# Performance work log

Measured on AMD Instinct MI355X. Metric: run time of the kernel, lower is better.

The kernel has to match this reference:

```python
import jax, jax.numpy as jnp
import numpy as np

B, S, D = 2, 2048, 1024
H = 16
HD = D // H  # 64
SCALE = HD ** -0.5
EPS = 1e-12  # F.normalize eps


def _rope_sin_cos(length, half, dtype):
    positions = jnp.arange(length, dtype=dtype)
    freqs = jnp.arange(half, dtype=dtype)
    inv_freq = 1.0 / 10000 ** (freqs / max(1, half))
    theta = jnp.einsum('s,f->sf', positions, inv_freq)  # [S, half]
    return jnp.sin(theta)[None, None], jnp.cos(theta)[None, None]  # [1,1,S,half]


def _rotate(x, sin, cos):
    # x: [B,H,S,HD]; interleaved even/odd rotation
    x_even = x[..., 0::2]
    x_odd = x[..., 1::2]
    r_even = x_even * cos - x_odd * sin
    r_odd = x_even * sin + x_odd * cos
    return jnp.stack([r_even, r_odd], axis=-1).reshape(x.shape)


def setup_inputs() -> dict:
    key = jax.random.key(0)
    k1, k2, k3 = jax.random.split(key, 3)
    tokens = jax.random.normal(k1, (B, S, D), dtype=jnp.float32)
    qkv_w = jax.random.normal(k2, (3 * D, D), dtype=jnp.float32) * (D ** -0.5)
    qkv_b = jnp.zeros((3 * D,), dtype=jnp.float32)
    out_w = jax.random.normal(k3, (D, D), dtype=jnp.float32) * (D ** -0.5)
    out_b = jnp.zeros((D,), dtype=jnp.float32)
    return {"tokens": tokens, "qkv_w": qkv_w, "qkv_b": qkv_b,
            "out_w": out_w, "out_b": out_b}


def reference(tokens, qkv_w, qkv_b, out_w, out_b):
    batch, length, _ = tokens.shape
    qkv = tokens @ qkv_w.T + qkv_b                       # [B,S,3D]
    qkv = qkv.reshape(batch, length, 3, H, HD)
    qkv = jnp.transpose(qkv, (0, 3, 1, 2, 4))            # [B,H,S,3,HD]
    q, k, v = qkv[..., 0, :], qkv[..., 1, :], qkv[..., 2, :]
    sin, cos = _rope_sin_cos(length, HD // 2, q.dtype)
    q = _rotate(q, sin, cos)
    k = _rotate(k, sin, cos)
    # QK L2-normalize (F.normalize: x / max(||x||, eps))
    q = q / jnp.maximum(jnp.linalg.norm(q, axis=-1, keepdims=True), EPS)
    k = k / jnp.maximum(jnp.linalg.norm(k, axis=-1, keepdims=True), EPS)
    scores = jnp.einsum('bhqd,bhkd->bhqk', q, k) * SCALE
    attn = jax.nn.softmax(scores, axis=-1)
    out = jnp.einsum('bhqk,bhkd->bhqd', attn, v)          # [B,H,S,HD]
    out = jnp.transpose(out, (0, 2, 1, 3)).reshape(batch, length, D)
    return out @ out_w.T + out_b
```

## Files before the change

kernel.cpp:

```cpp
#include <hip/hip_runtime.h>
#include <hip/hip_bf16.h>
#include <math.h>

#define B_ 2
#define S_ 2048
#define D_ 1024
#define H_ 16
#define HD_ 64
#define BHS (B_*H_*S_)
#define NROWS (B_*S_)

typedef __attribute__((ext_vector_type(8))) short bf16x8;
typedef __attribute__((ext_vector_type(4))) short bf16x4;
typedef __attribute__((ext_vector_type(4))) float f32x4;
typedef __attribute__((ext_vector_type(4))) int i32x4;

#ifdef __HIP_DEVICE_COMPILE__
#define EXP2(x) __builtin_amdgcn_exp2f(x)
#else
#define EXP2(x) exp2f(x)
#endif

#define MFMA32(a, b, c) __builtin_amdgcn_mfma_f32_16x16x32_bf16(a, b, c, 0, 0, 0)

#define SCALE_LOG2E 0.18033688011112043f

#define VMCNT(N) asm volatile("s_waitcnt vmcnt(" #N ")" ::: "memory")
#define SBAR() do { __builtin_amdgcn_s_barrier(); \
                    __builtin_amdgcn_sched_barrier(0); } while (0)

__device__ __forceinline__ short f2bf(float x) {
  __hip_bfloat16 h = __float2bfloat16(x);
  return *reinterpret_cast<short*>(&h);
}
__device__ __forceinline__ int packbf_hu(float lo, float hi) {
  unsigned lb = __float_as_uint(lo) + 0x8000u;
  unsigned hb = __float_as_uint(hi) + 0x8000u;
  return (int)__builtin_amdgcn_perm(hb, lb, 0x07060302u);
}

__device__ __forceinline__ void gload_lds16(const short* g, short* l) {
  __builtin_amdgcn_global_load_lds(
      (const __attribute__((address_space(1))) void*)g,
      (__attribute__((address_space(3))) void*)l, 16, 0, 0);
}

__global__ __launch_bounds__(256) void prep(
    const float* __restrict__ tokens, const float* __restrict__ qkv_w,
    const float* __restrict__ out_w, short* __restrict__ tok_bf,
    short* __restrict__ qkvw_bf, short* __restrict__ outw_bf,
    float* __restrict__ tab) {
  const int i = blockIdx.x * 256 + threadIdx.x;
  const float* src;
  short* dst;
  int j;
  if (i < 524288) {
    src = tokens; dst = tok_bf; j = i;
  } else if (i < 917504) {
    src = qkv_w; dst = qkvw_bf; j = i - 524288;
  } else if (i < 1048576) {
    src = out_w; dst = outw_bf; j = i - 917504;
  } else if (i < 1056768) {
    const int e = (i - 1048576) * 8;
    const int s = e >> 5;
    const int f0 = e & 31;
#pragma unroll
    for (int k = 0; k < 8; k++) {
      const int f = f0 + k;
      const float theta = (float)s * exp2f(-(float)f * 0.41524101186092034f);
      float sn, cs;
      sincosf(theta, &sn, &cs);
      tab[(s * 32 + f) * 2] = sn;
      tab[(s * 32 + f) * 2 + 1] = cs;
    }
    return;
  } else {
    return;
  }
  const float4 a = *(const float4*)(src + (long)j * 8);
  const float4 b = *(const float4*)(src + (long)j * 8 + 4);
  short tmp[8] = {f2bf(a.x), f2bf(a.y), f2bf(a.z), f2bf(a.w),
                  f2bf(b.x), f2bf(b.y), f2bf(b.z), f2bf(b.w)};
  *(bf16x8*)(dst + (long)j * 8) = *(const bf16x8*)tmp;
}

__global__ __launch_bounds__(256) void qkv_mfma(
    const short* __restrict__ A, const short* __restrict__ W,
    const float* __restrict__ bias, const float* __restrict__ tab,
    short* __restrict__ qb, short* __restrict__ kb, short* __restrict__ vtb) {
  __shared__ short smem[24576];
  const int t = threadIdx.x;
  const int w = t >> 6;
  const int lane = t & 63;
  const int col = lane & 15;
  const int quad = lane >> 4;
  const int wm = w >> 1;
  const int wn = w & 1;
  const int bid = blockIdx.x;
  const int xcd = bid & 7;
  const int seq = bid >> 3;
  const int m0 = (seq / 3) * 128;
  const int n0 = (xcd * 3 + seq % 3) * 128;

  f32x4 acc[4][4] = {};

  auto stage = [&](short* As, short* Bs, int k0) {
#pragma unroll
    for (int i = 0; i < 2; i++) {
      const int c0 = i * 256 + w * 64;
      const int c = c0 + lane;
      const int row = c >> 2;
      const int gseg = (c & 3) ^ ((row >> 1) & 3);
      gload_lds16(&A[(m0 + row) * 1024 + k0 + gseg * 8], As + c0 * 8);
    }
#pragma unroll
    for (int i = 0; i < 2; i++) {
      const int c0 = i * 256 + w * 64;
      const int c = c0 + lane;
      const int row = c >> 2;
      const int gseg = (c & 3) ^ ((row >> 1) & 3);
      gload_lds16(&W[(n0 + row) * 1024 + k0 + gseg * 8], Bs + c0 * 8);
    }
  };

  auto compute = [&](const short* As, const short* Bs) {
    bf16x8 af[4], bfr[4];
#pragma unroll
    for (int mt = 0; mt < 4; mt++) {
      const int m = wm * 64 + mt * 16 + col;
      af[mt] = *(const bf16x8*)&As[m * 32 + ((quad ^ ((m >> 1) & 3)) * 8)];
    }
#pragma unroll
    for (int nt = 0; nt < 4; nt++) {
      const int n = wn * 64 + nt * 16 + col;
      bfr[nt] = *(const bf16x8*)&Bs[n * 32 + ((quad ^ ((n >> 1) & 3)) * 8)];
    }
#pragma unroll
    for (int mt = 0; mt < 4; mt++)
#pragma unroll
      for (int nt = 0; nt < 4; nt++)
        acc[mt][nt] = MFMA32(af[mt], bfr[nt], acc[mt][nt]);
  };

  short* As0 = smem;          short* Bs0 = smem + 4096;
  short* As1 = smem + 8192;   short* Bs1 = smem + 12288;
  short* As2 = smem + 16384;  short* Bs2 = smem + 20480;

  stage(As0, Bs0, 0);
  stage(As1, Bs1, 32);
  for (int it = 0; it < 10; it++) {
    const int k = it * 96;
    VMCNT(4); SBAR(); stage(As2, Bs2, k + 64);  compute(As0, Bs0);
    VMCNT(4); SBAR(); stage(As0, Bs0, k + 96);  compute(As1, Bs1);
    VMCNT(4); SBAR(); stage(As1, Bs1, k + 128); compute(As2, Bs2);
  }
  VMCNT(4); SBAR(); compute(As0, Bs0);
  VMCNT(0); SBAR(); compute(As1, Bs1);
  __syncthreads();

  const int j_base = n0 + wn * 64;
  const int c = j_base >> 10;
  const int h = (j_base >> 6) & 15;
  float bi[4];
#pragma unroll
  for (int nt = 0; nt < 4; nt++) bi[nt] = bias[j_base + nt * 16 + col];

  if (c < 2) {
    short* dst = (c == 0) ? qb : kb;
    float* Tf = (float*)smem + w * 1088;
#pragma unroll
    for (int mt = 0; mt < 4; mt++) {
#pragma unroll
      for (int nt = 0; nt < 4; nt++)
#pragma unroll
        for (int r = 0; r < 4; r++)
          Tf[(quad * 4 + r) * 68 + nt * 16 + col] = acc[mt][nt][r] + bi[nt];
#pragma unroll
      for (int p = 0; p < 4; p++) {
        const int rloc = p * 4 + quad;
        const int n = m0 + wm * 64 + mt * 16 + rloc;
        const int bidx = n >> 11;
        const int s = n & 2047;
        const float4 xv = *(const float4*)&Tf[rloc * 68 + col * 4];
        const float4 tc = *(const float4*)&tab[s * 64 + col * 4];
        const float e0 = xv.x * tc.y - xv.y * tc.x;
        const float o0 = xv.x * tc.x + xv.y * tc.y;
        const float e1 = xv.z * tc.w - xv.w * tc.z;
        const float o1 = xv.z * tc.z + xv.w * tc.w;
        float ss = e0 * e0 + o0 * o0 + e1 * e1 + o1 * o1;
        ss += __shfl_xor(ss, 1, 64);
        ss += __shfl_xor(ss, 2, 64);
        ss += __shfl_xor(ss, 4, 64);
        ss += __shfl_xor(ss, 8, 64);
        float scl = 1.0f / fmaxf(sqrtf(ss), 1e-12f);
        if (c == 0) scl *= SCALE_LOG2E;
        int2 pk;
        pk.x = packbf_hu(e0 * scl, o0 * scl);
        pk.y = packbf_hu(e1 * scl, o1 * scl);
        *(int2*)&dst[((long)(bidx * 16 + h) * 2048 + s) * 64 + col * 4] = pk;
      }
    }
  } else {
    const int bidx = m0 >> 11;
    const int st = ((m0 & 2047) >> 6) + wm;
    short* vbase = vtb + ((long)(bidx * 16 + h) * 32 + st) * 4096;
#pragma unroll
    for (int mtp = 0; mtp < 2; mtp++)
#pragma unroll
      for (int ntq = 0; ntq < 4; ntq++) {
        int4 pk4;
        pk4.x = packbf_hu(acc[2 * mtp][ntq][0] + bi[ntq],
                          acc[2 * mtp][ntq][1] + bi[ntq]);
        pk4.y = packbf_hu(acc[2 * mtp][ntq][2] + bi[ntq],
                          acc[2 * mtp][ntq][3] + bi[ntq]);
        pk4.z = packbf_hu(acc[2 * mtp + 1][ntq][0] + bi[ntq],
                          acc[2 * mtp + 1][ntq][1] + bi[ntq]);
        pk4.w = packbf_hu(acc[2 * mtp + 1][ntq][2] + bi[ntq],
                          acc[2 * mtp + 1][ntq][3] + bi[ntq]);
        *(int4*)&vbase[(mtp * 4 + ntq) * 512 + quad * 128 + col * 8] = pk4;
      }
  }
}

__global__ __launch_bounds__(512) void attn_mfma(
    const short* __restrict__ qb,
    const short* __restrict__ kb,
    const short* __restrict__ vt,
    short* __restrict__ ob) {
  __shared__ __align__(16) char smem[65536];
  short* Ks = (short*)smem;
  short* Vs = Ks + 16384;
  const int t = threadIdx.x;
  const int w = t >> 6;
  const int grp = w >> 2;
  const int wl = w & 3;
  const int lane = t & 63;
  const int col = lane & 15;
  const int quad = lane >> 4;
  const int bh = blockIdx.x;
  const int q0 = blockIdx.y * 128;
  const long hb = (long)bh * S_ * 64;
  const short* kg = kb + hb;
  const short* vg = vt + (long)bh * 64 * S_;

  bf16x8 qa[2][2];
#pragma unroll
  for (int mt2 = 0; mt2 < 2; mt2++)
#pragma unroll
    for (int h = 0; h < 2; h++)
      qa[mt2][h] = *(const bf16x8*)&qb[hb +
          (long)(q0 + wl * 32 + mt2 * 16 + col) * 64 + h * 32 + quad * 8];

  const int tt = (wl << 6) | lane;
  int kofs[2];
#pragma unroll
  for (int i = 0; i < 2; i++) {
    const int cc = tt + 256 * i;
    kofs[i] = ((cc >> 7) * 16 + (cc & 15)) * 64 + ((cc >> 6) & 1) * 32 +
              ((cc >> 4) & 3) * 8;
  }

  short* KfL0 = Ks + grp * 4096;
  short* KfL1 = KfL0 + 8192;
  short* VfL0 = Vs + grp * 4096;
  short* VfL1 = VfL0 + 8192;

  f32x4 oacc[2][4] = {};
  f32x4 lacc[2] = {};
  const short oneb = 0x3F80;
  const bf16x8 ones8 = {oneb, oneb, oneb, oneb, oneb, oneb, oneb, oneb};

  auto stage = [&](short* KfL, short* VfL, int kt) {
    const short* kgp = kg + (long)kt * 64;
    const short* vgp = vg + (long)(kt >> 6) * 4096;
#pragma unroll
    for (int i = 0; i < 2; i++) {
      gload_lds16(kgp + kofs[i], KfL + i * 2048 + wl * 512);
      gload_lds16(vgp + (tt + 256 * i) * 8, VfL + i * 2048 + wl * 512);
    }
  };

  auto compute = [&](const short* KfL, const short* VfL) {
#pragma unroll
    for (int ntp = 0; ntp < 2; ntp++) {
      i32x4 pw[2];
#pragma unroll
      for (int half = 0; half < 2; half++) {
        const int nt = ntp * 2 + half;
        const bf16x8 ka0 =
            *(const bf16x8*)&KfL[nt * 1024 + quad * 128 + col * 8];
        const bf16x8 ka1 =
            *(const bf16x8*)&KfL[nt * 1024 + 512 + quad * 128 + col * 8];
#pragma unroll
        for (int mt2 = 0; mt2 < 2; mt2++) {
          f32x4 z = {0.f, 0.f, 0.f, 0.f};
          z = MFMA32(ka0, qa[mt2][0], z);
          z = MFMA32(ka1, qa[mt2][1], z);
          const float e0 = EXP2(z[0]);
          const float e1 = EXP2(z[1]);
          const float e2 = EXP2(z[2]);
          const float e3 = EXP2(z[3]);
          if (half == 0) {
            pw[mt2].x = packbf_hu(e0, e1);
            pw[mt2].y = packbf_hu(e2, e3);
          } else {
            pw[mt2].z = packbf_hu(e0, e1);
            pw[mt2].w = packbf_hu(e2, e3);
          }
        }
      }
      const bf16x8 pb0 = __builtin_bit_cast(bf16x8, pw[0]);
      const bf16x8 pb1 = __builtin_bit_cast(bf16x8, pw[1]);
      lacc[0] = MFMA32(ones8, pb0, lacc[0]);
      lacc[1] = MFMA32(ones8, pb1, lacc[1]);
#pragma unroll
      for (int dt = 0; dt < 4; dt++) {
        const bf16x8 va = *(const bf16x8*)
            &VfL[(ntp * 4 + dt) * 512 + quad * 128 + col * 8];
        oacc[0][dt] = MFMA32(va, pb0, oacc[0][dt]);
        oacc[1][dt] = MFMA32(va, pb1, oacc[1][dt]);
      }
    }
  };

  const int base = grp * 1024;
  stage(KfL0, VfL0, base);
  __syncthreads();
  for (int it = 0; it < 8; it++) {
    const int kt0 = base + it * 128;
    stage(KfL1, VfL1, kt0 + 64);
    compute(KfL0, VfL0);
    __syncthreads();
    if (it < 7) stage(KfL0, VfL0, kt0 + 128);
    compute(KfL1, VfL1);
    __syncthreads();
  }

  float* Ocomb = (float*)smem;
  float* lsumC = (float*)(smem + 34816);
  if (grp == 1) {
#pragma unroll
    for (int mt2 = 0; mt2 < 2; mt2++) {
      const int qloc = wl * 32 + mt2 * 16 + col;
      if (quad == 0) lsumC[qloc] = lacc[mt2][0];
#pragma unroll
      for (int dt = 0; dt < 4; dt++)
        *(f32x4*)&Ocomb[qloc * 68 + dt * 16 + quad * 4] = oacc[mt2][dt];
    }
  }
  __syncthreads();
  if (grp == 0) {
#pragma unroll
    for (int mt2 = 0; mt2 < 2; mt2++) {
      const int qloc = wl * 32 + mt2 * 16 + col;
      const float inv = 1.0f / (lacc[mt2][0] + lsumC[qloc]);
      short* orow = ob + hb + (long)(q0 + qloc) * 64;
#pragma unroll
      for (int dt = 0; dt < 4; dt++) {
        const float4 oc = *(const float4*)&Ocomb[qloc * 68 + dt * 16 + quad * 4];
        int2 pk;
        pk.x = packbf_hu((oacc[mt2][dt][0] + oc.x) * inv,
                         (oacc[mt2][dt][1] + oc.y) * inv);
        pk.y = packbf_hu((oacc[mt2][dt][2] + oc.z) * inv,
                         (oacc[mt2][dt][3] + oc.w) * inv);
        *(int2*)&orow[dt * 16 + quad * 4] = pk;
      }
    }
  }
}

__global__ __launch_bounds__(256) void out_mfma(
    const short* __restrict__ O, const short* __restrict__ W,
    const float* __restrict__ bias, float* __restrict__ out) {
  __shared__ short smem[12288];
  const int t = threadIdx.x;
  const int w = t >> 6;
  const int lane = t & 63;
  const int col = lane & 15;
  const int quad = lane >> 4;
  const int wm = w >> 1;
  const int wn = w & 1;
  const int bid = blockIdx.x;
  const int xcd = bid & 7;
  const int seq = bid >> 3;
  const int m0 = (seq >> 1) * 64;
  const int n0 = (xcd * 2 + (seq & 1)) * 64;

  f32x4 acc[2][2] = {};

  auto stage = [&](short* As, short* Bs, int k0) {
    {
      const int c = w * 64 + lane;
      const int row = c >> 2;
      const int gseg = (c & 3) ^ ((row >> 1) & 3);
      const int n = m0 + row;
      const int bidx = n >> 11;
      const int s = n & 2047;
      const int kk = k0 + gseg * 8;
      gload_lds16(&O[((long)(bidx * 16 + (kk >> 6)) * 2048 + s) * 64 + (kk & 63)],
                  As + w * 512);
    }
    {
      const int c = w * 64 + lane;
      const int row = c >> 2;
      const int gseg = (c & 3) ^ ((row >> 1) & 3);
      gload_lds16(&W[(n0 + row) * 1024 + k0 + gseg * 8], Bs + w * 512);
    }
  };

  auto compute = [&](const short* As, const short* Bs) {
    bf16x8 af[2], bfr[2];
#pragma unroll
    for (int mt = 0; mt < 2; mt++) {
      const int m = wm * 32 + mt * 16 + col;
      af[mt] = *(const bf16x8*)&As[m * 32 + ((quad ^ ((m >> 1) & 3)) * 8)];
    }
#pragma unroll
    for (int nt = 0; nt < 2; nt++) {
      const int n = wn * 32 + nt * 16 + col;
      bfr[nt] = *(const bf16x8*)&Bs[n * 32 + ((quad ^ ((n >> 1) & 3)) * 8)];
    }
#pragma unroll
    for (int mt = 0; mt < 2; mt++)
#pragma unroll
      for (int nt = 0; nt < 2; nt++)
        acc[mt][nt] = MFMA32(af[mt], bfr[nt], acc[mt][nt]);
  };

  short* As0 = smem;          short* Bs0 = smem + 2048;
  short* As1 = smem + 4096;   short* Bs1 = smem + 6144;
  short* As2 = smem + 8192;   short* Bs2 = smem + 10240;

  stage(As0, Bs0, 0);
  stage(As1, Bs1, 32);
  for (int it = 0; it < 10; it++) {
    const int k = it * 96;
    VMCNT(2); SBAR(); stage(As2, Bs2, k + 64);  compute(As0, Bs0);
    VMCNT(2); SBAR(); stage(As0, Bs0, k + 96);  compute(As1, Bs1);
    VMCNT(2); SBAR(); stage(As1, Bs1, k + 128); compute(As2, Bs2);
  }
  VMCNT(2); SBAR(); compute(As0, Bs0);
  VMCNT(0); SBAR(); compute(As1, Bs1);

  float bi[2];
#pragma unroll
  for (int nt = 0; nt < 2; nt++) bi[nt] = bias[n0 + wn * 32 + nt * 16 + col];
#pragma unroll
  for (int mt = 0; mt < 2; mt++) {
#pragma unroll
    for (int r = 0; r < 4; r++) {
      const int n = m0 + wm * 32 + mt * 16 + quad * 4 + r;
#pragma unroll
      for (int nt = 0; nt < 2; nt++)
        out[(long)n * 1024 + n0 + wn * 32 + nt * 16 + col] =
            acc[mt][nt][r] + bi[nt];
    }
  }
}

extern "C" void kernel_launch(void* const* d_in, const int* in_sizes, int n_in,
                              void* d_out, int out_size, void* d_ws,
                              size_t ws_size, hipStream_t stream) {
  const float* tokens = (const float*)d_in[0];
  const float* qkv_w = (const float*)d_in[1];
  const float* qkv_b = (const float*)d_in[2];
  const float* out_w = (const float*)d_in[3];
  const float* out_b = (const float*)d_in[4];
  float* out = (float*)d_out;

  const size_t per = (size_t)BHS * HD_;
  float* tab = (float*)d_ws;
  short* tok_bf = (short*)(tab + 2048 * 64);
  short* qkvw_bf = tok_bf + per;
  short* outw_bf = qkvw_bf + 3 * per / 4;
  short* q_bf = outw_bf + per / 4;
  short* k_bf = q_bf + per;
  short* vt_bf = k_bf + per;
  short* O_bf = vt_bf + per;

  hipLaunchKernelGGL(prep, dim3(4128), dim3(256), 0, stream, tokens, qkv_w,
                     out_w, tok_bf, qkvw_bf, outw_bf, tab);
  hipLaunchKernelGGL(qkv_mfma, dim3(768), dim3(256), 0, stream, tok_bf,
                     qkvw_bf, qkv_b, tab, q_bf, k_bf, vt_bf);
  hipLaunchKernelGGL(attn_mfma, dim3(B_ * H_, S_ / 128), dim3(512), 0, stream,
                     q_bf, k_bf, vt_bf, O_bf);
  hipLaunchKernelGGL(out_mfma, dim3(1024), dim3(256), 0, stream, O_bf,
                     outw_bf, out_b, out);
}
```

Measured before the change: 180.8 us.

## Replace LDS-staged GEMM pipelines with direct global-to-register fragment loads

Both projection GEMM kernels (qkv and output) drop their triple-buffered LDS staging with async global_load_lds and barriers. Each wave now loads its MFMA fragments straight from global memory into registers, double-buffered across a fully unrolled K loop. This removes LDS traffic and block-wide barriers, but gives up cross-wave operand sharing: each operand row is fetched by several waves through cache instead of once per block. It also uses more registers and relies on the compiler to overlap loads with MFMAs.

Measured after the change: 272.3 us. 50.6% more time.

```diff
diff --git a/kernel.cpp b/kernel.cpp
--- a/kernel.cpp
+++ b/kernel.cpp
@@ -24,10 +24,6 @@
 #define MFMA32(a, b, c) __builtin_amdgcn_mfma_f32_16x16x32_bf16(a, b, c, 0, 0, 0)
 
 #define SCALE_LOG2E 0.18033688011112043f
-
-#define VMCNT(N) asm volatile("s_waitcnt vmcnt(" #N ")" ::: "memory")
-#define SBAR() do { __builtin_amdgcn_s_barrier(); \
-                    __builtin_amdgcn_sched_barrier(0); } while (0)
 
 __device__ __forceinline__ short f2bf(float x) {
   __hip_bfloat16 h = __float2bfloat16(x);
@@ -88,7 +84,7 @@
     const short* __restrict__ A, const short* __restrict__ W,
     const float* __restrict__ bias, const float* __restrict__ tab,
     short* __restrict__ qb, short* __restrict__ kb, short* __restrict__ vtb) {
-  __shared__ short smem[24576];
+  __shared__ float Tf_s[4352];
   const int t = threadIdx.x;
   const int w = t >> 6;
   const int lane = t & 63;
@@ -102,61 +98,38 @@
   const int m0 = (seq / 3) * 128;
   const int n0 = (xcd * 3 + seq % 3) * 128;
 
+  const short* aB[4];
+  const short* bB[4];
+#pragma unroll
+  for (int mt = 0; mt < 4; mt++)
+    aB[mt] = A + (long)(m0 + wm * 64 + mt * 16 + col) * 1024 + quad * 8;
+#pragma unroll
+  for (int nt = 0; nt < 4; nt++)
+    bB[nt] = W + (long)(n0 + wn * 64 + nt * 16 + col) * 1024 + quad * 8;
+
   f32x4 acc[4][4] = {};
-
-  auto stage = [&](short* As, short* Bs, int k0) {
-#pragma unroll
-    for (int i = 0; i < 2; i++) {
-      const int c0 = i * 256 + w * 64;
-      const int c = c0 + lane;
-      const int row = c >> 2;
-      const int gseg = (c & 3) ^ ((row >> 1) & 3);
-      gload_lds16(&A[(m0 + row) * 1024 + k0 + gseg * 8], As + c0 * 8);
-    }
-#pragma unroll
-    for (int i = 0; i < 2; i++) {
-      const int c0 = i * 256 + w * 64;
-      const int c = c0 + lane;
-      const int row = c >> 2;
-      const int gseg = (c & 3) ^ ((row >> 1) & 3);
-      gload_lds16(&W[(n0 + row) * 1024 + k0 + gseg * 8], Bs + c0 * 8);
-    }
-  };
-
-  auto compute = [&](const short* As, const short* Bs) {
-    bf16x8 af[4], bfr[4];
-#pragma unroll
-    for (int mt = 0; mt < 4; mt++) {
-      const int m = wm * 64 + mt * 16 + col;
-      af[mt] = *(const bf16x8*)&As[m * 32 + ((quad ^ ((m >> 1) & 3)) * 8)];
-    }
-#pragma unroll
-    for (int nt = 0; nt < 4; nt++) {
-      const int n = wn * 64 + nt * 16 + col;
-      bfr[nt] = *(const bf16x8*)&Bs[n * 32 + ((quad ^ ((n >> 1) & 3)) * 8)];
+  bf16x8 fA[2][4], fB[2][4];
+#pragma unroll
+  for (int i = 0; i < 4; i++) {
+    fA[0][i] = *(const bf16x8*)(aB[i]);
+    fB[0][i] = *(const bf16x8*)(bB[i]);
+  }
+#pragma unroll
+  for (int s = 0; s < 32; s++) {
+    const int cur = s & 1, nxt = cur ^ 1;
+    if (s < 31) {
+#pragma unroll
+      for (int i = 0; i < 4; i++) {
+        fA[nxt][i] = *(const bf16x8*)(aB[i] + (s + 1) * 32);
+        fB[nxt][i] = *(const bf16x8*)(bB[i] + (s + 1) * 32);
+      }
     }
 #pragma unroll
     for (int mt = 0; mt < 4; mt++)
 #pragma unroll
       for (int nt = 0; nt < 4; nt++)
-        acc[mt][nt] = MFMA32(af[mt], bfr[nt], acc[mt][nt]);
-  };
-
-  short* As0 = smem;          short* Bs0 = smem + 4096;
-  short* As1 = smem + 8192;   short* Bs1 = smem + 12288;
-  short* As2 = smem + 16384;  short* Bs2 = smem + 20480;
-
-  stage(As0, Bs0, 0);
-  stage(As1, Bs1, 32);
-  for (int it = 0; it < 10; it++) {
-    const int k = it * 96;
-    VMCNT(4); SBAR(); stage(As2, Bs2, k + 64);  compute(As0, Bs0);
-    VMCNT(4); SBAR(); stage(As0, Bs0, k + 96);  compute(As1, Bs1);
-    VMCNT(4); SBAR(); stage(As1, Bs1, k + 128); compute(As2, Bs2);
-  }
-  VMCNT(4); SBAR(); compute(As0, Bs0);
-  VMCNT(0); SBAR(); compute(As1, Bs1);
-  __syncthreads();
+        acc[mt][nt] = MFMA32(fA[cur][mt], fB[cur][nt], acc[mt][nt]);
+  }
 
   const int j_base = n0 + wn * 64;
   const int c = j_base >> 10;
@@ -167,7 +140,7 @@
 
   if (c < 2) {
     short* dst = (c == 0) ? qb : kb;
-    float* Tf = (float*)smem + w * 1088;
+    float* Tf = Tf_s + w * 1088;
 #pragma unroll
     for (int mt = 0; mt < 4; mt++) {
 #pragma unroll
@@ -372,7 +345,6 @@
 __global__ __launch_bounds__(256) void out_mfma(
     const short* __restrict__ O, const short* __restrict__ W,
     const float* __restrict__ bias, float* __restrict__ out) {
-  __shared__ short smem[12288];
   const int t = threadIdx.x;
   const int w = t >> 6;
   const int lane = t & 63;
@@ -386,61 +358,43 @@
   const int m0 = (seq >> 1) * 64;
   const int n0 = (xcd * 2 + (seq & 1)) * 64;
 
+  const short* aB[2];
+#pragma unroll
+  for (int mt = 0; mt < 2; mt++) {
+    const int n = m0 + wm * 32 + mt * 16 + col;
+    const int bidx = n >> 11;
+    const int srow = n & 2047;
+    aB[mt] = O + ((long)(bidx * 16) * 2048 + srow) * 64 + quad * 8;
+  }
+  const short* bB[2];
+#pragma unroll
+  for (int nt = 0; nt < 2; nt++)
+    bB[nt] = W + (long)(n0 + wn * 32 + nt * 16 + col) * 1024 + quad * 8;
+
   f32x4 acc[2][2] = {};
-
-  auto stage = [&](short* As, short* Bs, int k0) {
-    {
-      const int c = w * 64 + lane;
-      const int row = c >> 2;
-      const int gseg = (c & 3) ^ ((row >> 1) & 3);
-      const int n = m0 + row;
-      const int bidx = n >> 11;
-      const int s = n & 2047;
-      const int kk = k0 + gseg * 8;
-      gload_lds16(&O[((long)(bidx * 16 + (kk >> 6)) * 2048 + s) * 64 + (kk & 63)],
-                  As + w * 512);
-    }
-    {
-      const int c = w * 64 + lane;
-      const int row = c >> 2;
-      const int gseg = (c & 3) ^ ((row >> 1) & 3);
-      gload_lds16(&W[(n0 + row) * 1024 + k0 + gseg * 8], Bs + w * 512);
-    }
-  };
-
-  auto compute = [&](const short* As, const short* Bs) {
-    bf16x8 af[2], bfr[2];
-#pragma unroll
-    for (int mt = 0; mt < 2; mt++) {
-      const int m = wm * 32 + mt * 16 + col;
-      af[mt] = *(const bf16x8*)&As[m * 32 + ((quad ^ ((m >> 1) & 3)) * 8)];
-    }
-#pragma unroll
-    for (int nt = 0; nt < 2; nt++) {
-      const int n = wn * 32 + nt * 16 + col;
-      bfr[nt] = *(const bf16x8*)&Bs[n * 32 + ((quad ^ ((n >> 1) & 3)) * 8)];
+  bf16x8 fA[2][2], fB[2][2];
+#pragma unroll
+  for (int i = 0; i < 2; i++) {
+    fA[0][i] = *(const bf16x8*)(aB[i]);
+    fB[0][i] = *(const bf16x8*)(bB[i]);
+  }
+#pragma unroll
+  for (int s = 0; s < 32; s++) {
+    const int cur = s & 1, nxt = cur ^ 1;
+    if (s < 31) {
+      const long ofsA = (long)((s + 1) >> 1) * 131072 + ((s + 1) & 1) * 32;
+#pragma unroll
+      for (int i = 0; i < 2; i++) {
+        fA[nxt][i] = *(const bf16x8*)(aB[i] + ofsA);
+        fB[nxt][i] = *(const bf16x8*)(bB[i] + (s + 1) * 32);
+      }
     }
 #pragma unroll
     for (int mt = 0; mt < 2; mt++)
 #pragma unroll
       for (int nt = 0; nt < 2; nt++)
-        acc[mt][nt] = MFMA32(af[mt], bfr[nt], acc[mt][nt]);
-  };
-
-  short* As0 = smem;          short* Bs0 = smem + 2048;
-  short* As1 = smem + 4096;   short* Bs1 = smem + 6144;
-  short* As2 = smem + 8192;   short* Bs2 = smem + 10240;
-
-  stage(As0, Bs0, 0);
-  stage(As1, Bs1, 32);
-  for (int it = 0; it < 10; it++) {
-    const int k = it * 96;
-    VMCNT(2); SBAR(); stage(As2, Bs2, k + 64);  compute(As0, Bs0);
-    VMCNT(2); SBAR(); stage(As0, Bs0, k + 96);  compute(As1, Bs1);
-    VMCNT(2); SBAR(); stage(As1, Bs1, k + 128); compute(As2, Bs2);
-  }
-  VMCNT(2); SBAR(); compute(As0, Bs0);
-  VMCNT(0); SBAR(); compute(As1, Bs1);
+        acc[mt][nt] = MFMA32(fA[cur][mt], fB[cur][nt], acc[mt][nt]);
+  }
 
   float bi[2];
 #pragma unroll
```
